# Kernel optimization log

Measured on AMD Instinct MI355X. Metric: run time of the kernel, lower is better.

## Reference

```python
import jax, jax.numpy as jnp
import numpy as np
import math

ALPHA = 0.5
GAMMA_ALPHA = math.gamma(ALPHA)

def _xavier(key, fan_in, fan_out):
    limit = math.sqrt(6.0 / (fan_in + fan_out))
    return jax.random.uniform(key, (fan_in, fan_out), jnp.float32, -limit, limit)

def setup_inputs() -> dict:
    key = jax.random.key(0)
    ks = jax.random.split(key, 8)
    B, T, D_IN, H, D_OUT = 512, 1024, 64, 256, 64
    x = jax.random.normal(ks[0], (B, D_IN), jnp.float32)
    t = jnp.arange(T, dtype=jnp.float32) * 0.01  # increasing time grid
    W0 = _xavier(ks[1], D_IN + 1, H); b0 = jnp.zeros((H,), jnp.float32)
    W1 = _xavier(ks[2], H, H);        b1 = jnp.zeros((H,), jnp.float32)
    W2 = _xavier(ks[3], H, H);        b2 = jnp.zeros((H,), jnp.float32)
    W3 = _xavier(ks[4], H, D_OUT);    b3 = jnp.zeros((D_OUT,), jnp.float32)
    return {"x": x, "t": t, "W0": W0, "b0": b0, "W1": W1, "b1": b1,
            "W2": W2, "b2": b2, "W3": W3, "b3": b3}

def reference(x, t, W0, b0, W1, b1, W2, b2, W3, b3):
    # Fractional Euler: y_i = y_{i-1} + (dt^alpha / Gamma(alpha)) * tanh(MLP([t_{i-1}, y_{i-1}]))
    B = x.shape[0]
    y0 = x  # input_dim == output_dim, so initial state is x directly
    t_prev = t[:-1]            # [T-1]
    dt = t[1:] - t[:-1]        # [T-1]

    def mlp(tp, state):
        h = jnp.concatenate([jnp.full((B, 1), tp, dtype=state.dtype), state], axis=-1)
        h = h @ W0 + b0
        h = h @ W1 + b1  # nn.Sequential has no activations between linears
        h = h @ W2 + b2
        h = h @ W3 + b3
        return jnp.tanh(h)  # single tanh applied in ode_func

    def step(state, inputs):
        tp, d = inputs
        deriv = mlp(tp, state)
        factor = (d ** ALPHA) / GAMMA_ALPHA
        new = state + factor * deriv
        return new, new

    _, traj = jax.lax.scan(step, y0, (t_prev, dt))   # traj: [T-1, B, D_OUT]
    solution = jnp.concatenate([y0[:, None, :], jnp.swapaxes(traj, 0, 1)], axis=1)
    return solution  # [B, T, D_OUT]
```

## Files before the change

kernel.cpp:

```cpp
#include <hip/hip_runtime.h>
#include <math.h>

#define HDIM 256
#define DDIM 64
#define BROWS 512
#define TSTEPS 1024
#define AROWS 66

typedef float f32x2 __attribute__((ext_vector_type(2)));
typedef float f32x4 __attribute__((ext_vector_type(4)));

__global__ void compose1(const float* __restrict__ W0, const float* __restrict__ b0,
                         const float* __restrict__ W1, const float* __restrict__ b1,
                         float* __restrict__ out1) {
    int r = blockIdx.x;
    int c = threadIdx.x;
    const float* arow = (r < 65) ? (W0 + r * HDIM) : b0;
    float acc = (r == 65) ? b1[c] : 0.0f;
    for (int h = 0; h < HDIM; ++h)
        acc = fmaf(arow[h], W1[h * HDIM + c], acc);
    out1[r * HDIM + c] = acc;
}

__global__ void compose2(const float* __restrict__ in1,
                         const float* __restrict__ W2, const float* __restrict__ b2,
                         float* __restrict__ out2) {
    int r = blockIdx.x, c = threadIdx.x;
    const float* arow = in1 + r * HDIM;
    float acc = (r == 65) ? b2[c] : 0.0f;
    for (int h = 0; h < HDIM; ++h)
        acc = fmaf(arow[h], W2[h * HDIM + c], acc);
    out2[r * HDIM + c] = acc;
}

__global__ void compose3(const float* __restrict__ in2,
                         const float* __restrict__ W3, const float* __restrict__ b3,
                         float* __restrict__ out3) {
    int r = blockIdx.x, c = threadIdx.x;
    const float* arow = in2 + r * HDIM;
    float acc = (r == 65) ? b3[c] : 0.0f;
    for (int h = 0; h < HDIM; ++h)
        acc = fmaf(arow[h], W3[h * DDIM + c], acc);
    out3[r * DDIM + c] = acc;
}

__device__ __forceinline__ void pkfma(f32x2& acc, f32x2 a, f32x2 b) {
    asm("v_pk_fma_f32 %0, %1, %2, %0" : "+v"(acc) : "v"(a), "v"(b));
}

__launch_bounds__(64, 1)
__global__ void fode_scan(const float* __restrict__ x, const float* __restrict__ t,
                          const float* __restrict__ Weff,
                          float* __restrict__ out) {
    const int b = blockIdx.x;
    const int d = threadIdx.x;

    __shared__ float  ylds[DDIM];
    __shared__ float2 plds[TSTEPS];

    const float invG = 0.56418958354775628695f;

    for (int i = d; i < TSTEPS - 1; i += DDIM) {
        float t0 = t[i];
        float t1 = t[i + 1];
        plds[i] = make_float2(t0, sqrtf(t1 - t0) * invG);
    }

    f32x2 Wp[DDIM / 2];
#pragma unroll
    for (int c = 0; c < DDIM / 2; ++c) {
        Wp[c].x = Weff[(1 + 2 * c) * DDIM + d];
        Wp[c].y = Weff[(2 + 2 * c) * DDIM + d];
    }
    const float wt   = Weff[d];
    const float bias = Weff[65 * DDIM + d];

    float y = x[b * DDIM + d];
    float* op = out + (size_t)b * TSTEPS * DDIM + d;
    *op = y;
    ylds[d] = y;
    asm volatile("" ::: "memory");

    float2 prm = plds[0];

    for (int k = 0; k < TSTEPS - 1; ++k) {
        f32x4 yv[16];
#pragma unroll
        for (int c = 0; c < 16; ++c)
            yv[c] = *reinterpret_cast<const f32x4*>(&ylds[c * 4]);

        float2 prm_next = plds[k + 1];
        float base = fmaf(prm.x, wt, bias);

        f32x2 acc0 = {0.f, 0.f}, acc1 = {0.f, 0.f};
#pragma unroll
        for (int c = 0; c < 16; ++c) {
            f32x2 lo = __builtin_shufflevector(yv[c], yv[c], 0, 1);
            f32x2 hi = __builtin_shufflevector(yv[c], yv[c], 2, 3);
            pkfma(acc0, lo, Wp[2 * c + 0]);
            pkfma(acc1, hi, Wp[2 * c + 1]);
        }
        float s = ((acc0.x + acc0.y) + (acc1.x + acc1.y)) + base;

        float e  = __builtin_amdgcn_exp2f(s * 2.88539008177792681472f);
        float th = fmaf(-2.0f, __builtin_amdgcn_rcpf(e + 1.0f), 1.0f);

        y = fmaf(prm.y, th, y);

        ylds[d] = y;
        asm volatile("" ::: "memory");
        op += DDIM;
        *op = y;
        prm = prm_next;
    }
}

extern "C" void kernel_launch(void* const* d_in, const int* in_sizes, int n_in,
                              void* d_out, int out_size, void* d_ws, size_t ws_size,
                              hipStream_t stream) {
    const float* x  = (const float*)d_in[0];
    const float* t  = (const float*)d_in[1];
    const float* W0 = (const float*)d_in[2];
    const float* b0 = (const float*)d_in[3];
    const float* W1 = (const float*)d_in[4];
    const float* b1 = (const float*)d_in[5];
    const float* W2 = (const float*)d_in[6];
    const float* b2 = (const float*)d_in[7];
    const float* W3 = (const float*)d_in[8];
    const float* b3 = (const float*)d_in[9];
    float* out = (float*)d_out;

    float* buf1 = (float*)d_ws;
    float* buf2 = buf1 + AROWS * HDIM;
    float* buf3 = buf2 + AROWS * HDIM;

    compose1<<<AROWS, HDIM, 0, stream>>>(W0, b0, W1, b1, buf1);
    compose2<<<AROWS, HDIM, 0, stream>>>(buf1, W2, b2, buf2);
    compose3<<<AROWS, DDIM, 0, stream>>>(buf2, W3, b3, buf3);
    fode_scan<<<BROWS, DDIM, 0, stream>>>(x, t, buf3, out);
}
```

Measured before the change: 286.2 us.

## Broadcast state across wavefront with permlane/DPP instead of LDS round-trip

Replaces the per-step LDS write and 16 vector LDS reads of the 64-element state with an in-register all-gather built from permlane32/16 swaps and DPP mirror/xor moves. The weight registers are permuted at setup to match the gathered lane order, and four accumulators replace two. The goal is to take LDS latency off the serial time-step dependency chain. In exchange each step runs about 60 extra DPP and permlane instructions, and the ds_bpermute fallback would add LDS traffic again if the swap builtins are missing.

```diff
diff --git a/kernel.cpp b/kernel.cpp
--- a/kernel.cpp
+++ b/kernel.cpp
@@ -8,7 +8,6 @@
 #define AROWS 66
 
 typedef float f32x2 __attribute__((ext_vector_type(2)));
-typedef float f32x4 __attribute__((ext_vector_type(4)));
 
 __global__ void compose1(const float* __restrict__ W0, const float* __restrict__ b0,
                          const float* __restrict__ W1, const float* __restrict__ b1,
@@ -48,6 +47,55 @@
     asm("v_pk_fma_f32 %0, %1, %2, %0" : "+v"(acc) : "v"(a), "v"(b));
 }
 
+#define DPP_QP_XOR1 0xB1
+#define DPP_QP_XOR2 0x4E
+#define DPP_ROW_MIRROR 0x140
+#define DPP_ROW_HALF_MIRROR 0x141
+
+template <int CTRL>
+__device__ __forceinline__ unsigned dpp_mov(unsigned v) {
+    return (unsigned)__builtin_amdgcn_update_dpp(0, (int)v, CTRL, 0xF, 0xF, true);
+}
+
+__device__ __forceinline__ void gather32(unsigned v, unsigned q[32]) {
+    unsigned t0, t1;
+#if __has_builtin(__builtin_amdgcn_permlane32_swap)
+    {
+        auto s = __builtin_amdgcn_permlane32_swap((int)v, (int)v, false, false);
+        t0 = (unsigned)s[0]; t1 = (unsigned)s[1];
+    }
+#else
+    t0 = v;
+    t1 = (unsigned)__builtin_amdgcn_ds_bpermute(
+            (int)(((threadIdx.x ^ 32u) & 63u) << 2), (int)v);
+#endif
+    unsigned u[4];
+#if __has_builtin(__builtin_amdgcn_permlane16_swap)
+    {
+        auto s = __builtin_amdgcn_permlane16_swap((int)t0, (int)t0, false, false);
+        u[0] = (unsigned)s[0]; u[1] = (unsigned)s[1];
+    }
+    {
+        auto s = __builtin_amdgcn_permlane16_swap((int)t1, (int)t1, false, false);
+        u[2] = (unsigned)s[0]; u[3] = (unsigned)s[1];
+    }
+#else
+    {
+        int a16 = (int)(((threadIdx.x ^ 16u) & 63u) << 2);
+        u[0] = t0; u[1] = (unsigned)__builtin_amdgcn_ds_bpermute(a16, (int)t0);
+        u[2] = t1; u[3] = (unsigned)__builtin_amdgcn_ds_bpermute(a16, (int)t1);
+    }
+#endif
+    unsigned w[8];
+#pragma unroll
+    for (int i = 0; i < 4; ++i) { w[i] = u[i]; w[4 + i] = dpp_mov<DPP_ROW_MIRROR>(u[i]); }
+    unsigned xx[16];
+#pragma unroll
+    for (int i = 0; i < 8; ++i) { xx[i] = w[i]; xx[8 + i] = dpp_mov<DPP_ROW_HALF_MIRROR>(w[i]); }
+#pragma unroll
+    for (int i = 0; i < 16; ++i) { q[i] = xx[i]; q[16 + i] = dpp_mov<DPP_QP_XOR2>(xx[i]); }
+}
+
 __launch_bounds__(64, 1)
 __global__ void fode_scan(const float* __restrict__ x, const float* __restrict__ t,
                           const float* __restrict__ Weff,
@@ -55,22 +103,26 @@
     const int b = blockIdx.x;
     const int d = threadIdx.x;
 
-    __shared__ float  ylds[DDIM];
     __shared__ float2 plds[TSTEPS];
 
     const float invG = 0.56418958354775628695f;
 
     for (int i = d; i < TSTEPS - 1; i += DDIM) {
-        float t0 = t[i];
-        float t1 = t[i + 1];
-        plds[i] = make_float2(t0, sqrtf(t1 - t0) * invG);
-    }
-
-    f32x2 Wp[DDIM / 2];
-#pragma unroll
-    for (int c = 0; c < DDIM / 2; ++c) {
-        Wp[c].x = Weff[(1 + 2 * c) * DDIM + d];
-        Wp[c].y = Weff[(2 + 2 * c) * DDIM + d];
+        float t0v = t[i];
+        float t1v = t[i + 1];
+        plds[i] = make_float2(t0v, sqrtf(t1v - t0v) * invG);
+    }
+
+    unsigned sig[32];
+    gather32((unsigned)d, sig);
+
+    f32x2 Wp[32];
+#pragma unroll
+    for (int c = 0; c < 32; ++c) {
+        unsigned j0 = sig[c];
+        unsigned j1 = dpp_mov<DPP_QP_XOR1>(sig[c]);
+        Wp[c].x = Weff[(1 + j0) * DDIM + d];
+        Wp[c].y = Weff[(1 + j1) * DDIM + d];
     }
     const float wt   = Weff[d];
     const float bias = Weff[65 * DDIM + d];
@@ -78,37 +130,46 @@
     float y = x[b * DDIM + d];
     float* op = out + (size_t)b * TSTEPS * DDIM + d;
     *op = y;
-    ylds[d] = y;
-    asm volatile("" ::: "memory");
 
     float2 prm = plds[0];
 
     for (int k = 0; k < TSTEPS - 1; ++k) {
-        f32x4 yv[16];
-#pragma unroll
-        for (int c = 0; c < 16; ++c)
-            yv[c] = *reinterpret_cast<const f32x4*>(&ylds[c * 4]);
-
         float2 prm_next = plds[k + 1];
+
+        unsigned q[32];
+        gather32(__float_as_uint(y), q);
+
         float base = fmaf(prm.x, wt, bias);
-
-        f32x2 acc0 = {0.f, 0.f}, acc1 = {0.f, 0.f};
-#pragma unroll
-        for (int c = 0; c < 16; ++c) {
-            f32x2 lo = __builtin_shufflevector(yv[c], yv[c], 0, 1);
-            f32x2 hi = __builtin_shufflevector(yv[c], yv[c], 2, 3);
-            pkfma(acc0, lo, Wp[2 * c + 0]);
-            pkfma(acc1, hi, Wp[2 * c + 1]);
+        f32x2 acc0 = {base, 0.f};
+        f32x2 acc1 = {0.f, 0.f};
+        f32x2 acc2 = {0.f, 0.f};
+        f32x2 acc3 = {0.f, 0.f};
+#pragma unroll
+        for (int c = 0; c < 32; c += 4) {
+            f32x2 p0, p1, p2, p3;
+            p0.x = __uint_as_float(q[c + 0]);
+            p0.y = __uint_as_float(dpp_mov<DPP_QP_XOR1>(q[c + 0]));
+            p1.x = __uint_as_float(q[c + 1]);
+            p1.y = __uint_as_float(dpp_mov<DPP_QP_XOR1>(q[c + 1]));
+            p2.x = __uint_as_float(q[c + 2]);
+            p2.y = __uint_as_float(dpp_mov<DPP_QP_XOR1>(q[c + 2]));
+            p3.x = __uint_as_float(q[c + 3]);
+            p3.y = __uint_as_float(dpp_mov<DPP_QP_XOR1>(q[c + 3]));
+            pkfma(acc0, p0, Wp[c + 0]);
+            pkfma(acc1, p1, Wp[c + 1]);
+            pkfma(acc2, p2, Wp[c + 2]);
+            pkfma(acc3, p3, Wp[c + 3]);
         }
-        float s = ((acc0.x + acc0.y) + (acc1.x + acc1.y)) + base;
+        f32x2 accA = acc0 + acc1;
+        f32x2 accB = acc2 + acc3;
+        f32x2 accT = accA + accB;
+        float s = accT.x + accT.y;
 
         float e  = __builtin_amdgcn_exp2f(s * 2.88539008177792681472f);
         float th = fmaf(-2.0f, __builtin_amdgcn_rcpf(e + 1.0f), 1.0f);
 
         y = fmaf(prm.y, th, y);
 
-        ylds[d] = y;
-        asm volatile("" ::: "memory");
         op += DDIM;
         *op = y;
         prm = prm_next;
```

After: 322.3 us. +12.6%, slower.

## Split state broadcast between cross-lane permutes and LDS reads in scan loop

Applied to the files above, without the earlier changes.

Each step's 64-wide state vector is no longer read entirely from LDS. Half of the elements now come from the lane's own half of the wave through permlane32/16 swaps and DPP moves, each lane getting a permuted order with the weights reordered to match. Only the other 32 elements are read from LDS. The aim is to shorten the per-step serial latency chain through the LDS write-then-read, at the cost of more VALU permute instructions and scalar FMAs instead of packed FMAs.

```diff
diff --git a/kernel.cpp b/kernel.cpp
--- a/kernel.cpp
+++ b/kernel.cpp
@@ -48,6 +48,37 @@
     asm("v_pk_fma_f32 %0, %1, %2, %0" : "+v"(acc) : "v"(a), "v"(b));
 }
 
+#define DPP_QP_XOR1 0xB1
+#define DPP_QP_XOR2 0x4E
+#define DPP_ROW_MIRROR 0x140
+#define DPP_ROW_HALF_MIRROR 0x141
+
+template <int CTRL>
+__device__ __forceinline__ unsigned dpp_mov(unsigned v) {
+    return (unsigned)__builtin_amdgcn_update_dpp(0, (int)v, CTRL, 0xF, 0xF, true);
+}
+
+__device__ __forceinline__ void gather_half(unsigned v, unsigned q[32]) {
+    unsigned A;
+    {
+        auto s = __builtin_amdgcn_permlane32_swap((int)v, (int)v, false, false);
+        A = (unsigned)s[0];
+    }
+    {
+        auto s = __builtin_amdgcn_permlane16_swap((int)A, (int)A, false, false);
+        q[0] = (unsigned)s[0];
+        q[1] = (unsigned)s[1];
+    }
+    q[2] = dpp_mov<DPP_QP_XOR1>(q[0]);
+    q[3] = dpp_mov<DPP_QP_XOR1>(q[1]);
+#pragma unroll
+    for (int i = 0; i < 4; ++i)  q[4 + i]  = dpp_mov<DPP_QP_XOR2>(q[i]);
+#pragma unroll
+    for (int i = 0; i < 8; ++i)  q[8 + i]  = dpp_mov<DPP_ROW_HALF_MIRROR>(q[i]);
+#pragma unroll
+    for (int i = 0; i < 16; ++i) q[16 + i] = dpp_mov<DPP_ROW_MIRROR>(q[i]);
+}
+
 __launch_bounds__(64, 1)
 __global__ void fode_scan(const float* __restrict__ x, const float* __restrict__ t,
                           const float* __restrict__ Weff,
@@ -66,11 +97,20 @@
         plds[i] = make_float2(t0, sqrtf(t1 - t0) * invG);
     }
 
-    f32x2 Wp[DDIM / 2];
+    unsigned sig[32];
+    gather_half((unsigned)d, sig);
+
+    float Wv[32];
 #pragma unroll
-    for (int c = 0; c < DDIM / 2; ++c) {
-        Wp[c].x = Weff[(1 + 2 * c) * DDIM + d];
-        Wp[c].y = Weff[(2 + 2 * c) * DDIM + d];
+    for (int c = 0; c < 32; ++c)
+        Wv[c] = Weff[(1 + (int)sig[c]) * DDIM + d];
+
+    const int dsj0 = (sig[0] < 32u) ? 32 : 0;
+    f32x2 Wd[16];
+#pragma unroll
+    for (int c = 0; c < 16; ++c) {
+        Wd[c].x = Weff[(1 + dsj0 + 2 * c + 0) * DDIM + d];
+        Wd[c].y = Weff[(1 + dsj0 + 2 * c + 1) * DDIM + d];
     }
     const float wt   = Weff[d];
     const float bias = Weff[65 * DDIM + d];
@@ -84,23 +124,35 @@
     float2 prm = plds[0];
 
     for (int k = 0; k < TSTEPS - 1; ++k) {
-        f32x4 yv[16];
+        float2 prm_next = plds[k + 1];
+
+        f32x4 yv[8];
 #pragma unroll
-        for (int c = 0; c < 16; ++c)
-            yv[c] = *reinterpret_cast<const f32x4*>(&ylds[c * 4]);
+        for (int c = 0; c < 8; ++c)
+            yv[c] = *reinterpret_cast<const f32x4*>(&ylds[dsj0 + 4 * c]);
 
-        float2 prm_next = plds[k + 1];
-        float base = fmaf(prm.x, wt, bias);
+        unsigned q[32];
+        gather_half(__float_as_uint(y), q);
 
-        f32x2 acc0 = {0.f, 0.f}, acc1 = {0.f, 0.f};
+        float a0 = fmaf(prm.x, wt, bias), a1 = 0.f, a2 = 0.f, a3 = 0.f;
 #pragma unroll
-        for (int c = 0; c < 16; ++c) {
+        for (int c = 0; c < 32; c += 4) {
+            a0 = fmaf(__uint_as_float(q[c + 0]), Wv[c + 0], a0);
+            a1 = fmaf(__uint_as_float(q[c + 1]), Wv[c + 1], a1);
+            a2 = fmaf(__uint_as_float(q[c + 2]), Wv[c + 2], a2);
+            a3 = fmaf(__uint_as_float(q[c + 3]), Wv[c + 3], a3);
+        }
+
+        f32x2 dacc0 = {0.f, 0.f}, dacc1 = {0.f, 0.f};
+#pragma unroll
+        for (int c = 0; c < 8; ++c) {
             f32x2 lo = __builtin_shufflevector(yv[c], yv[c], 0, 1);
             f32x2 hi = __builtin_shufflevector(yv[c], yv[c], 2, 3);
-            pkfma(acc0, lo, Wp[2 * c + 0]);
-            pkfma(acc1, hi, Wp[2 * c + 1]);
+            pkfma(dacc0, lo, Wd[2 * c + 0]);
+            pkfma(dacc1, hi, Wd[2 * c + 1]);
         }
-        float s = ((acc0.x + acc0.y) + (acc1.x + acc1.y)) + base;
+        f32x2 dd = dacc0 + dacc1;
+        float s = ((a0 + a1) + (a2 + a3)) + (dd.x + dd.y);
 
         float e  = __builtin_amdgcn_exp2f(s * 2.88539008177792681472f);
         float th = fmaf(-2.0f, __builtin_amdgcn_rcpf(e + 1.0f), 1.0f);
```

Result: slower. 318.0 us, median of 2 (+11.1%).

## Update pre-activation incrementally via tanh products and split dot across half-waves

Applied to the files above, without the earlier changes.

The MLP collapses to an affine map, so the scan now keeps the pre-activation s and updates it as s += dt*w_t + factor*(W·tanh), writing th instead of y to LDS. The state-dependent dot product no longer waits on the y update. Each half-wave reads only half of the 64-element vector and computes partial sums for two output columns, combined with permlane32_swap, which halves the LDS read volume. The exp scale constant is folded into the weights, and inline asm with partial lgkmcnt waits overlaps the LDS reads with the FMAs. In exchange, s accumulates rounding error over the steps instead of being recomputed from y each time.

```diff
diff --git a/kernel.cpp b/kernel.cpp
--- a/kernel.cpp
+++ b/kernel.cpp
@@ -55,64 +55,142 @@
     const int b = blockIdx.x;
     const int d = threadIdx.x;
 
-    __shared__ float  ylds[DDIM];
-    __shared__ float2 plds[TSTEPS];
+    __shared__ __align__(16) float ylds[DDIM];
+    __shared__ __align__(8) float2 plds[TSTEPS];
 
     const float invG = 0.56418958354775628695f;
+    const float K2L = 2.88539008177792681472f;
 
     for (int i = d; i < TSTEPS - 1; i += DDIM) {
         float t0 = t[i];
         float t1 = t[i + 1];
-        plds[i] = make_float2(t0, sqrtf(t1 - t0) * invG);
-    }
-
-    f32x2 Wp[DDIM / 2];
+        float dt = t1 - t0;
+        plds[i] = make_float2(dt, sqrtf(dt) * invG);
+    }
+
+    const int lo = d & 31;
+    const int hh = d >> 5;
+
+    f32x2 Wa[16], Wb[16];
 #pragma unroll
-    for (int c = 0; c < DDIM / 2; ++c) {
-        Wp[c].x = Weff[(1 + 2 * c) * DDIM + d];
-        Wp[c].y = Weff[(2 + 2 * c) * DDIM + d];
-    }
-    const float wt   = Weff[d];
-    const float bias = Weff[65 * DDIM + d];
+    for (int c = 0; c < 16; ++c) {
+        int j = 32 * hh + 2 * c;
+        Wa[c].x = K2L * Weff[(1 + j) * DDIM + lo];
+        Wa[c].y = K2L * Weff[(2 + j) * DDIM + lo];
+        Wb[c].x = K2L * Weff[(1 + j) * DDIM + lo + 32];
+        Wb[c].y = K2L * Weff[(2 + j) * DDIM + lo + 32];
+    }
+    const float wts   = K2L * Weff[d];
+    const float biass = K2L * Weff[65 * DDIM + d];
+
+    auto cal = __builtin_amdgcn_permlane32_swap(d, d, false, false);
+    const bool pick0 = (cal[0] == (d ^ 32));
+
+    const unsigned ybase = (unsigned)(uintptr_t)&ylds[0];
+    const unsigned waddr = ybase + 4u * (unsigned)d;
+    const unsigned rbase = ybase + 128u * (unsigned)hh;
+    const unsigned pbase = (unsigned)(uintptr_t)&plds[0];
+
+    const float t0g = t[0];
 
     float y = x[b * DDIM + d];
     float* op = out + (size_t)b * TSTEPS * DDIM + d;
     *op = y;
-    ylds[d] = y;
-    asm volatile("" ::: "memory");
-
-    float2 prm = plds[0];
+
+#define READS8(r0,r1,r2,r3,r4,r5,r6,r7)                                   \
+    asm volatile(                                                         \
+        "ds_read_b128 %[o0], %[a] offset:0\n\t"                           \
+        "ds_read_b128 %[o1], %[a] offset:16\n\t"                          \
+        "ds_read_b128 %[o2], %[a] offset:32\n\t"                          \
+        "ds_read_b128 %[o3], %[a] offset:48\n\t"                          \
+        "ds_read_b128 %[o4], %[a] offset:64\n\t"                          \
+        "ds_read_b128 %[o5], %[a] offset:80\n\t"                          \
+        "ds_read_b128 %[o6], %[a] offset:96\n\t"                          \
+        "ds_read_b128 %[o7], %[a] offset:112"                             \
+        : [o0] "=&v"(r0), [o1] "=&v"(r1), [o2] "=&v"(r2), [o3] "=&v"(r3), \
+          [o4] "=&v"(r4), [o5] "=&v"(r5), [o6] "=&v"(r6), [o7] "=&v"(r7)  \
+        : [a] "v"(rbase))
+
+#define QUADH(vq, c)                                                      \
+    {                                                                     \
+        f32x2 qlo = __builtin_shufflevector(vq, vq, 0, 1);                \
+        f32x2 qhi = __builtin_shufflevector(vq, vq, 2, 3);                \
+        pkfma(accA0, qlo, Wa[2 * (c) + 0]);                               \
+        pkfma(accA1, qhi, Wa[2 * (c) + 1]);                               \
+        pkfma(accB0, qlo, Wb[2 * (c) + 0]);                               \
+        pkfma(accB1, qhi, Wb[2 * (c) + 1]);                               \
+    }
+
+    float s;
+    {
+        asm volatile("ds_write_b32 %0, %1" :: "v"(waddr), "v"(y));
+        f32x4 v0, v1, v2, v3, v4, v5, v6, v7;
+        READS8(v0, v1, v2, v3, v4, v5, v6, v7);
+        float base0 = fmaf(t0g, wts, biass);
+        asm volatile("s_waitcnt lgkmcnt(0)" ::: "memory");
+        __builtin_amdgcn_sched_barrier(0);
+        f32x2 accA0 = {0.f, 0.f}, accA1 = {0.f, 0.f};
+        f32x2 accB0 = {0.f, 0.f}, accB1 = {0.f, 0.f};
+        QUADH(v0, 0) QUADH(v1, 1) QUADH(v2, 2) QUADH(v3, 3)
+        QUADH(v4, 4) QUADH(v5, 5) QUADH(v6, 6) QUADH(v7, 7)
+        f32x2 ra = accA0 + accA1;  float qa = ra.x + ra.y;
+        f32x2 rb = accB0 + accB1;  float qb = rb.x + rb.y;
+        float keep = (d < 32) ? qa : qb;
+        float send = (d < 32) ? qb : qa;
+        auto sw = __builtin_amdgcn_permlane32_swap(__float_as_int(send),
+                                                   __float_as_int(send), false, false);
+        float recv = __int_as_float(pick0 ? sw[0] : sw[1]);
+        s = base0 + (keep + recv);
+    }
+
+    f32x2 prm;
+    prm.x = plds[0].x;
+    prm.y = plds[0].y;
 
     for (int k = 0; k < TSTEPS - 1; ++k) {
-        f32x4 yv[16];
-#pragma unroll
-        for (int c = 0; c < 16; ++c)
-            yv[c] = *reinterpret_cast<const f32x4*>(&ylds[c * 4]);
-
-        float2 prm_next = plds[k + 1];
-        float base = fmaf(prm.x, wt, bias);
-
-        f32x2 acc0 = {0.f, 0.f}, acc1 = {0.f, 0.f};
-#pragma unroll
-        for (int c = 0; c < 16; ++c) {
-            f32x2 lo = __builtin_shufflevector(yv[c], yv[c], 0, 1);
-            f32x2 hi = __builtin_shufflevector(yv[c], yv[c], 2, 3);
-            pkfma(acc0, lo, Wp[2 * c + 0]);
-            pkfma(acc1, hi, Wp[2 * c + 1]);
-        }
-        float s = ((acc0.x + acc0.y) + (acc1.x + acc1.y)) + base;
-
-        float e  = __builtin_amdgcn_exp2f(s * 2.88539008177792681472f);
+        float e  = __builtin_amdgcn_exp2f(s);
         float th = fmaf(-2.0f, __builtin_amdgcn_rcpf(e + 1.0f), 1.0f);
+        asm volatile("ds_write_b32 %0, %1" :: "v"(waddr), "v"(th));
+
+        f32x4 v0, v1, v2, v3, v4, v5, v6, v7;
+        READS8(v0, v1, v2, v3, v4, v5, v6, v7);
+        f32x2 prmn;
+        unsigned paddr = pbase + 8u * (unsigned)(k + 1);
+        asm volatile("ds_read_b64 %0, %1" : "=&v"(prmn) : "v"(paddr));
 
         y = fmaf(prm.y, th, y);
-
-        ylds[d] = y;
-        asm volatile("" ::: "memory");
         op += DDIM;
         *op = y;
-        prm = prm_next;
-    }
+        float sc = fmaf(prm.x, wts, s);
+
+        f32x2 accA0 = {0.f, 0.f}, accA1 = {0.f, 0.f};
+        f32x2 accB0 = {0.f, 0.f}, accB1 = {0.f, 0.f};
+
+        asm volatile("s_waitcnt lgkmcnt(5)" ::: "memory");
+        __builtin_amdgcn_sched_barrier(0);
+        QUADH(v0, 0) QUADH(v1, 1) QUADH(v2, 2) QUADH(v3, 3)
+
+        asm volatile("s_waitcnt lgkmcnt(1)" ::: "memory");
+        __builtin_amdgcn_sched_barrier(0);
+        QUADH(v4, 4) QUADH(v5, 5) QUADH(v6, 6) QUADH(v7, 7)
+
+        f32x2 ra = accA0 + accA1;  float qa = ra.x + ra.y;
+        f32x2 rb = accB0 + accB1;  float qb = rb.x + rb.y;
+        float keep = (d < 32) ? qa : qb;
+        float send = (d < 32) ? qb : qa;
+        auto sw = __builtin_amdgcn_permlane32_swap(__float_as_int(send),
+                                                   __float_as_int(send), false, false);
+        float recv = __int_as_float(pick0 ? sw[0] : sw[1]);
+        float dotT = keep + recv;
+
+        s = fmaf(prm.y, dotT, sc);
+
+        asm volatile("s_waitcnt lgkmcnt(0)" ::: "memory");
+        __builtin_amdgcn_sched_barrier(0);
+        prm = prmn;
+    }
+#undef QUADH
+#undef READS8
 }
 
 extern "C" void kernel_launch(void* const* d_in, const int* in_sizes, int n_in,
```

Result: faster. 237.5 us (-17.0%).
